# Optimization experiments

Hardware: AMD Instinct MI355X
Metric: run time of the kernel (lower is better)

## Reference

```python
import jax, jax.numpy as jnp
import numpy as np

D_MODEL = 1024
NUM_HEADS = 16
HEAD_DIM = D_MODEL // NUM_HEADS


def setup_inputs() -> dict:
    key = jax.random.key(0)
    k1, k2, k3, k4, k5 = jax.random.split(key, 5)
    scale = 1.0 / np.sqrt(D_MODEL)
    x = jax.random.normal(k1, (2, 2048, D_MODEL), dtype=jnp.float32)
    Wqkv = jax.random.uniform(k2, (D_MODEL, 3 * D_MODEL), jnp.float32, -scale, scale)
    bqkv = jax.random.uniform(k3, (3 * D_MODEL,), jnp.float32, -scale, scale)
    Wout = jax.random.uniform(k4, (D_MODEL, D_MODEL), jnp.float32, -scale, scale)
    bout = jax.random.uniform(k5, (D_MODEL,), jnp.float32, -scale, scale)
    return {"x": x, "Wqkv": Wqkv, "bqkv": bqkv, "Wout": Wout, "bout": bout}


def reference(x, Wqkv, bqkv, Wout, bout):
    B, S, _ = x.shape
    qkv = x @ Wqkv + bqkv                                   # [B, S, 3*D]
    # reshape to [B, S, H, 3*head_dim] then to [B, H, S, 3*head_dim]
    qkv = qkv.reshape(B, S, NUM_HEADS, 3 * HEAD_DIM).transpose(0, 2, 1, 3)
    q, k, v = jnp.split(qkv, 3, axis=-1)                    # each [B, H, S, hd]
    scaled = jnp.einsum("bhqd,bhkd->bhqk", q, k) / jnp.sqrt(jnp.float32(HEAD_DIM))
    attn = jax.nn.softmax(scaled, axis=-1)                  # [B, H, S, S]
    values = jnp.einsum("bhqk,bhkd->bhqd", attn, v)         # [B, H, S, hd]
    values = values.transpose(0, 2, 1, 3).reshape(B, S, D_MODEL)
    return values @ Wout + bout
```

## Files before the change

### kernel.cpp

```cpp
#include <hip/hip_runtime.h>


typedef __attribute__((ext_vector_type(8)))  short short8;
typedef __attribute__((ext_vector_type(4)))  short short4v;
typedef __attribute__((ext_vector_type(8)))  float float8;
typedef __attribute__((ext_vector_type(4)))  float f32x4;
typedef __attribute__((ext_vector_type(16))) float f32x16;
typedef __attribute__((ext_vector_type(4)))  int   int4v;

#define D_MODEL 1024
#define NHEAD   16
#define HD      64
#define SEQ     2048
#define N3      (3*D_MODEL)
#define MB      (1024*1024)

static __device__ __forceinline__ float bf2f(short s) {
    unsigned u = ((unsigned)(unsigned short)s) << 16;
    return __builtin_bit_cast(float, u);
}
static __device__ __forceinline__ short f2bf(float f) {
    unsigned u = __builtin_bit_cast(unsigned, f);
    u = (u + 0x7fff + ((u >> 16) & 1)) >> 16;
    return (short)u;
}
static __device__ __forceinline__ unsigned cvtpk(float a, float b) {
    unsigned r;
    asm("v_cvt_pk_bf16_f32 %0, %1, %2" : "=v"(r) : "v"(a), "v"(b));
    return r;
}
#define PLSWAP(a, b) asm("v_permlane32_swap_b32 %0, %1" : "+v"(a), "+v"(b))

static __device__ __forceinline__ void gl16(const short* g, short* l) {
    __builtin_amdgcn_global_load_lds(
        (const __attribute__((address_space(1))) unsigned int*)g,
        (__attribute__((address_space(3))) unsigned int*)l, 16, 0, 0);
}

__global__ __launch_bounds__(256) void prep(
    const float* __restrict__ x, const float* __restrict__ Wqkv,
    const float* __restrict__ Wout,
    short* __restrict__ Xh, short* __restrict__ Xl,
    short* __restrict__ Wh, short* __restrict__ Wl,
    short* __restrict__ Woh, short* __restrict__ Wol)
{
    __shared__ float tile[32][33];
    const int bid = blockIdx.x;
    const int tid = threadIdx.x;

    if (bid < 2048) {
        const int i = (bid * 256 + tid) * 8;
        const float8 v = *(const float8*)&x[i];
        short8 h, l;
#pragma unroll
        for (int j = 0; j < 8; ++j) {
            h[j] = f2bf(v[j]);
            l[j] = f2bf(v[j] - bf2f(h[j]));
        }
        *(short8*)&Xh[i] = h;
        *(short8*)&Xl[i] = l;
        return;
    }

    const float* in; short *hi, *lo; int K, N, bx, by;
    if (bid < 5120) {
        const int b2 = bid - 2048;
        in = Wqkv; hi = Wh; lo = Wl; K = D_MODEL; N = N3;
        bx = b2 % 96; by = b2 / 96;
    } else {
        const int b3 = bid - 5120;
        in = Wout; hi = Woh; lo = Wol; K = D_MODEL; N = D_MODEL;
        bx = b3 & 31; by = b3 >> 5;
    }
    const int n0 = bx * 32, k0 = by * 32;
    const int tx = tid & 31, ty = tid >> 5;
#pragma unroll
    for (int i = 0; i < 4; ++i)
        tile[ty + 8*i][tx] = in[(k0 + ty + 8*i) * N + (n0 + tx)];
    __syncthreads();
#pragma unroll
    for (int i = 0; i < 4; ++i) {
        const float v  = tile[tx][ty + 8*i];
        const short vh = f2bf(v);
        const short vl = f2bf(v - bf2f(vh));
        const int idx  = (n0 + ty + 8*i) * K + (k0 + tx);
        hi[idx] = vh;
        lo[idx] = vl;
    }
}

#define QBUF_SH 20480
#define OFF_AL  4096
#define OFF_BH  8192
#define OFF_BL  14336

__global__ __launch_bounds__(512, 4) void qkv_gemm8(
    const short* __restrict__ Xh, const short* __restrict__ Xl,
    const short* __restrict__ Bh, const short* __restrict__ Bl,
    const float* __restrict__ bias,
    short* __restrict__ Qo, short* __restrict__ Ko, short* __restrict__ Vt)
{
    __shared__ __attribute__((aligned(16))) short smem[2 * QBUF_SH];

    const int tid  = threadIdx.x;
    const int wave = tid >> 6, lane = tid & 63;
    const int q4 = lane >> 4, l16 = lane & 15;
    const int wr = wave >> 2, wc = wave & 3;
    const int csw = (q4 ^ ((l16 ^ (l16 >> 2)) & 3)) * 8;

    const int flat = blockIdx.x;
    const int sw = (flat & 7) * 64 + (flat >> 3);
    const int mt = sw & 31, nt = sw >> 5;
    const int m0 = mt * 128, n0 = nt * 192;

    const short* srcp[5];
#pragma unroll
    for (int j = 0; j < 5; ++j) {
        const int id = j * 512 + tid;
        int r; const short* mat; int row0;
        if (id < 512)       { r = id >> 2;          mat = Xh; row0 = m0; }
        else if (id < 1024) { r = (id - 512) >> 2;  mat = Xl; row0 = m0; }
        else if (id < 1792) { r = (id - 1024) >> 2; mat = Bh; row0 = n0; }
        else                { r = (id - 1792) >> 2; mat = Bl; row0 = n0; }
        const int cg = (id & 3) ^ ((r ^ (r >> 2)) & 3);
        srcp[j] = &mat[(size_t)(row0 + r) * D_MODEL + cg * 8];
    }

    auto stage = [&](int b) {
#pragma unroll
        for (int j = 0; j < 5; ++j) {
            gl16(srcp[j], smem + b * QBUF_SH + (j * 512 + tid) * 8);
            srcp[j] += 32;
        }
    };

    f32x4 acc[4][3];
#pragma unroll
    for (int i = 0; i < 4; ++i)
#pragma unroll
        for (int j = 0; j < 3; ++j) acc[i][j] = (f32x4){0.f, 0.f, 0.f, 0.f};

    stage(0);
    asm volatile("s_waitcnt vmcnt(0)" ::: "memory");
    __builtin_amdgcn_s_barrier();

    for (int t = 0; t < 32; ++t) {
        const int cur = t & 1;
        const short* base = smem + cur * QBUF_SH;
        const short* Ah_s = base;
        const short* Al_s = base + OFF_AL;
        const short* Bh_s = base + OFF_BH;
        const short* Bl_s = base + OFF_BL;

        short8 bhf[3], blf[3], a0h[2], a0l[2];
#pragma unroll
        for (int n = 0; n < 3; ++n) {
            const int rb = (wc * 48 + n * 16 + l16) * 32 + csw;
            bhf[n] = *(const short8*)(Bh_s + rb);
            blf[n] = *(const short8*)(Bl_s + rb);
        }
#pragma unroll
        for (int ti = 0; ti < 2; ++ti) {
            const int ra = (wr * 64 + ti * 16 + l16) * 32 + csw;
            a0h[ti] = *(const short8*)(Ah_s + ra);
            a0l[ti] = *(const short8*)(Al_s + ra);
        }
        if (t < 31) stage(cur ^ 1);
        __builtin_amdgcn_s_barrier();
        asm volatile("s_waitcnt lgkmcnt(0)" ::: "memory");
        __builtin_amdgcn_sched_barrier(0);
        short8 a1h[2], a1l[2];
#pragma unroll
        for (int ti = 0; ti < 2; ++ti) {
            const int ra = (wr * 64 + (2 + ti) * 16 + l16) * 32 + csw;
            a1h[ti] = *(const short8*)(Ah_s + ra);
            a1l[ti] = *(const short8*)(Al_s + ra);
        }
        __builtin_amdgcn_sched_barrier(0);
        __builtin_amdgcn_s_setprio(1);
#pragma unroll
        for (int ti = 0; ti < 2; ++ti)
#pragma unroll
            for (int n = 0; n < 3; ++n) {
                acc[ti][n] = __builtin_amdgcn_mfma_f32_16x16x32_bf16(a0h[ti], bhf[n], acc[ti][n], 0, 0, 0);
                acc[ti][n] = __builtin_amdgcn_mfma_f32_16x16x32_bf16(a0h[ti], blf[n], acc[ti][n], 0, 0, 0);
                acc[ti][n] = __builtin_amdgcn_mfma_f32_16x16x32_bf16(a0l[ti], bhf[n], acc[ti][n], 0, 0, 0);
            }
        __builtin_amdgcn_s_setprio(0);
        __builtin_amdgcn_s_barrier();

        asm volatile("s_waitcnt lgkmcnt(0)" ::: "memory");
        __builtin_amdgcn_sched_barrier(0);
        __builtin_amdgcn_s_setprio(1);
#pragma unroll
        for (int ti = 0; ti < 2; ++ti)
#pragma unroll
            for (int n = 0; n < 3; ++n) {
                acc[2+ti][n] = __builtin_amdgcn_mfma_f32_16x16x32_bf16(a1h[ti], bhf[n], acc[2+ti][n], 0, 0, 0);
                acc[2+ti][n] = __builtin_amdgcn_mfma_f32_16x16x32_bf16(a1h[ti], blf[n], acc[2+ti][n], 0, 0, 0);
                acc[2+ti][n] = __builtin_amdgcn_mfma_f32_16x16x32_bf16(a1l[ti], bhf[n], acc[2+ti][n], 0, 0, 0);
            }
        __builtin_amdgcn_s_setprio(0);
        asm volatile("s_waitcnt vmcnt(0)" ::: "memory");
        __builtin_amdgcn_s_barrier();
    }

    const float SCALE_Q = 0.125f * 1.4426950408889634f;
#pragma unroll
    for (int tj = 0; tj < 3; ++tj) {
        const int jj = wc * 48 + tj * 16 + l16;
        const int n  = nt * 192 + jj;
        const float bv = bias[n];
#pragma unroll
        for (int ti = 0; ti < 4; ++ti) {
            const int mb = m0 + wr * 64 + ti * 16 + q4 * 4;
            const int b = mb >> 11;
            const int s = mb & 2047;
            const int bh_ = b * NHEAD + nt;
            if (jj >= 128) {
                short4v v4;
#pragma unroll
                for (int r = 0; r < 4; ++r) v4[r] = f2bf(acc[ti][tj][r] + bv);
                *(short4v*)&Vt[(bh_ * HD + (jj - 128)) * SEQ + s] = v4;
            } else if (jj < 64) {
#pragma unroll
                for (int r = 0; r < 4; ++r)
                    Qo[(bh_ * SEQ + s + r) * HD + jj] = f2bf((acc[ti][tj][r] + bv) * SCALE_Q);
            } else {
#pragma unroll
                for (int r = 0; r < 4; ++r)
                    Ko[(bh_ * SEQ + s + r) * HD + (jj - 64)] = f2bf(acc[ti][tj][r] + bv);
            }
        }
    }
}

__global__ __launch_bounds__(256, 2) void attn_tscore(
    const short* __restrict__ Q, const short* __restrict__ K,
    const short* __restrict__ Vt,
    float* __restrict__ Opart, float2* __restrict__ Ml)
{
    __shared__ __attribute__((aligned(16))) char smem[36864];
    short (*Ks)[72] = (short(*)[72])smem;
    short (*Vs)[72] = (short(*)[72])(smem + 18432);

    const int bh  = blockIdx.x;
    const int qb  = blockIdx.y;
    const int kvz = blockIdx.z;

    const short* Qp  = Q  + (size_t)bh * SEQ * HD;
    const short* Kp  = K  + (size_t)bh * SEQ * HD + (size_t)kvz * 1024 * HD;
    const short* Vtp = Vt + (size_t)bh * HD * SEQ + (size_t)kvz * 1024;

    const int tid  = threadIdx.x;
    const int wave = tid >> 6, lane = tid & 63;
    const int l5 = lane & 31, hf = lane >> 5;
    const int q0w = qb * 128 + wave * 32;

    short8 qf[4];
#pragma unroll
    for (int c = 0; c < 4; ++c)
        qf[c] = *(const short8*)&Qp[(q0w + l5) * HD + c * 16 + hf * 8];

    f32x16 oacc0 = (f32x16)(0.f), oacc1 = (f32x16)(0.f);
    float m = -1.0e30f, l = 0.f;

    const int sr = tid >> 2;
    const int sc = (tid & 3) * 16;

    short8 kr0 = *(const short8*)&Kp[sr * HD + sc];
    short8 kr1 = *(const short8*)&Kp[sr * HD + sc + 8];
    short8 vr0 = *(const short8*)&Vtp[sr * SEQ + sc];
    short8 vr1 = *(const short8*)&Vtp[sr * SEQ + sc + 8];
    *(short8*)&Ks[sr][sc]     = kr0;
    *(short8*)&Ks[sr][sc + 8] = kr1;
    *(short8*)&Vs[sr][sc]     = vr0;
    *(short8*)&Vs[sr][sc + 8] = vr1;
    __syncthreads();

    for (int kc = 0; kc < 16; ++kc) {
        const int buf = (kc & 1) << 6;

        if (kc < 15) {
            const int nkb = (kc + 1) << 6;
            kr0 = *(const short8*)&Kp[(nkb + sr) * HD + sc];
            kr1 = *(const short8*)&Kp[(nkb + sr) * HD + sc + 8];
            vr0 = *(const short8*)&Vtp[sr * SEQ + nkb + sc];
            vr1 = *(const short8*)&Vtp[sr * SEQ + nkb + sc + 8];
        }

        f32x16 s0 = (f32x16)(0.f), s1 = (f32x16)(0.f);
#pragma unroll
        for (int c = 0; c < 4; ++c) {
            const short8 ka0 = *(const short8*)&Ks[buf + l5][c * 16 + hf * 8];
            const short8 ka1 = *(const short8*)&Ks[buf + 32 + l5][c * 16 + hf * 8];
            s0 = __builtin_amdgcn_mfma_f32_32x32x16_bf16(ka0, qf[c], s0, 0, 0, 0);
            s1 = __builtin_amdgcn_mfma_f32_32x32x16_bf16(ka1, qf[c], s1, 0, 0, 0);
        }

        float t[8];
#pragma unroll
        for (int i = 0; i < 8; ++i)
            t[i] = fmaxf(fmaxf(s0[i], s0[i + 8]), fmaxf(s1[i], s1[i + 8]));
        float pmax = fmaxf(fmaxf(fmaxf(t[0], t[1]), fmaxf(t[2], t[3])),
                           fmaxf(fmaxf(t[4], t[5]), fmaxf(t[6], t[7])));
        pmax = fmaxf(pmax, __shfl_xor(pmax, 32, 64));

        if (!__all(pmax - m <= 8.0f)) {
            const float mnew  = fmaxf(m, pmax);
            const float alpha = exp2f(m - mnew);
#pragma unroll
            for (int i = 0; i < 16; ++i) { oacc0[i] *= alpha; oacc1[i] *= alpha; }
            l *= alpha;
            m = mnew;
        }

        float p0[16], p1[16];
#pragma unroll
        for (int i = 0; i < 16; ++i) { p0[i] = exp2f(s0[i] - m); p1[i] = exp2f(s1[i] - m); }
        float sa = 0.f, sb = 0.f, sc_ = 0.f, sd = 0.f;
#pragma unroll
        for (int i = 0; i < 4; ++i) {
            sa += p0[i] + p0[i + 8];
            sb += p0[i + 4] + p0[i + 12];
            sc_ += p1[i] + p1[i + 8];
            sd += p1[i + 4] + p1[i + 12];
        }
        float rs = (sa + sb) + (sc_ + sd);
        rs += __shfl_xor(rs, 32, 64);
        l += rs;

        unsigned u0 = cvtpk(p0[0],  p0[1]),  u1 = cvtpk(p0[2],  p0[3]);
        unsigned u2 = cvtpk(p0[4],  p0[5]),  u3 = cvtpk(p0[6],  p0[7]);
        unsigned u4 = cvtpk(p0[8],  p0[9]),  u5 = cvtpk(p0[10], p0[11]);
        unsigned u6 = cvtpk(p0[12], p0[13]), u7 = cvtpk(p0[14], p0[15]);
        unsigned w0 = cvtpk(p1[0],  p1[1]),  w1 = cvtpk(p1[2],  p1[3]);
        unsigned w2 = cvtpk(p1[4],  p1[5]),  w3 = cvtpk(p1[6],  p1[7]);
        unsigned w4 = cvtpk(p1[8],  p1[9]),  w5 = cvtpk(p1[10], p1[11]);
        unsigned w6 = cvtpk(p1[12], p1[13]), w7 = cvtpk(p1[14], p1[15]);
        PLSWAP(u0, u2); PLSWAP(u1, u3); PLSWAP(u4, u6); PLSWAP(u5, u7);
        PLSWAP(w0, w2); PLSWAP(w1, w3); PLSWAP(w4, w6); PLSWAP(w5, w7);
        int4v pb0 = (int4v){ (int)u0, (int)u1, (int)u2, (int)u3 };
        int4v pb1 = (int4v){ (int)u4, (int)u5, (int)u6, (int)u7 };
        int4v pb2 = (int4v){ (int)w0, (int)w1, (int)w2, (int)w3 };
        int4v pb3 = (int4v){ (int)w4, (int)w5, (int)w6, (int)w7 };
        const short8 pbf0 = __builtin_bit_cast(short8, pb0);
        const short8 pbf1 = __builtin_bit_cast(short8, pb1);
        const short8 pbf2 = __builtin_bit_cast(short8, pb2);
        const short8 pbf3 = __builtin_bit_cast(short8, pb3);

        {
            const short8 va0 = *(const short8*)&Vs[buf + l5][hf * 8];
            const short8 va1 = *(const short8*)&Vs[buf + l5][16 + hf * 8];
            const short8 va2 = *(const short8*)&Vs[buf + l5][32 + hf * 8];
            const short8 va3 = *(const short8*)&Vs[buf + l5][48 + hf * 8];
            oacc0 = __builtin_amdgcn_mfma_f32_32x32x16_bf16(va0, pbf0, oacc0, 0, 0, 0);
            oacc0 = __builtin_amdgcn_mfma_f32_32x32x16_bf16(va1, pbf1, oacc0, 0, 0, 0);
            oacc0 = __builtin_amdgcn_mfma_f32_32x32x16_bf16(va2, pbf2, oacc0, 0, 0, 0);
            oacc0 = __builtin_amdgcn_mfma_f32_32x32x16_bf16(va3, pbf3, oacc0, 0, 0, 0);
            const short8 vb0 = *(const short8*)&Vs[buf + 32 + l5][hf * 8];
            const short8 vb1 = *(const short8*)&Vs[buf + 32 + l5][16 + hf * 8];
            const short8 vb2 = *(const short8*)&Vs[buf + 32 + l5][32 + hf * 8];
            const short8 vb3 = *(const short8*)&Vs[buf + 32 + l5][48 + hf * 8];
            oacc1 = __builtin_amdgcn_mfma_f32_32x32x16_bf16(vb0, pbf0, oacc1, 0, 0, 0);
            oacc1 = __builtin_amdgcn_mfma_f32_32x32x16_bf16(vb1, pbf1, oacc1, 0, 0, 0);
            oacc1 = __builtin_amdgcn_mfma_f32_32x32x16_bf16(vb2, pbf2, oacc1, 0, 0, 0);
            oacc1 = __builtin_amdgcn_mfma_f32_32x32x16_bf16(vb3, pbf3, oacc1, 0, 0, 0);
        }

        if (kc < 15) {
            const int wb = ((kc + 1) & 1) << 6;
            *(short8*)&Ks[wb + sr][sc]     = kr0;
            *(short8*)&Ks[wb + sr][sc + 8] = kr1;
            *(short8*)&Vs[wb + sr][sc]     = vr0;
            *(short8*)&Vs[wb + sr][sc + 8] = vr1;
        }
        __syncthreads();
    }

    float* Op = Opart + ((((size_t)kvz * 32 + bh) * 16 + qb) * 4 + wave) * 2048;
#pragma unroll
    for (int r = 0; r < 4; ++r) {
        float4 v;
        v.x = oacc0[4*r]; v.y = oacc0[4*r+1]; v.z = oacc0[4*r+2]; v.w = oacc0[4*r+3];
        *(float4*)&Op[r * 256 + lane * 4] = v;
    }
#pragma unroll
    for (int r = 0; r < 4; ++r) {
        float4 v;
        v.x = oacc1[4*r]; v.y = oacc1[4*r+1]; v.z = oacc1[4*r+2]; v.w = oacc1[4*r+3];
        *(float4*)&Op[(4 + r) * 256 + lane * 4] = v;
    }
    if (hf == 0) {
        float2 mv; mv.x = m; mv.y = l;
        Ml[((size_t)kvz * 32 + bh) * 2048 + q0w + l5] = mv;
    }
}

__global__ __launch_bounds__(256) void attn_merge(
    const float* __restrict__ Opart, const float2* __restrict__ Ml,
    short* __restrict__ Ch, short* __restrict__ Cl)
{
    __shared__ float epi[4][32][68];
    const int tid = threadIdx.x, wave = tid >> 6, lane = tid & 63;
    const int l5 = lane & 31, hf = lane >> 5;
    const int task = blockIdx.x * 4 + wave;
    const int bh = task >> 6;
    const int qb = (task >> 2) & 15;
    const int wq = task & 3;
    const int bi = bh >> 4, hi_ = bh & 15;
    const int q0w = qb * 128 + wq * 32;

    const float2 v0 = Ml[(size_t)bh * 2048 + q0w + l5];
    const float2 v1 = Ml[((size_t)32 + bh) * 2048 + q0w + l5];
    const float M  = fmaxf(v0.x, v1.x);
    const float w0 = exp2f(v0.x - M), w1 = exp2f(v1.x - M);
    const float inv = 1.0f / (v0.y * w0 + v1.y * w1);
    const float f0 = w0 * inv, f1 = w1 * inv;

    const float* Op0 = Opart + (((size_t)bh * 16 + qb) * 4 + wq) * 2048;
    const float* Op1 = Opart + ((((size_t)32 + bh) * 16 + qb) * 4 + wq) * 2048;
    float o[32];
#pragma unroll
    for (int r = 0; r < 8; ++r) {
        const float4 a = *(const float4*)&Op0[r * 256 + lane * 4];
        const float4 b = *(const float4*)&Op1[r * 256 + lane * 4];
        o[4*r]   = a.x * f0 + b.x * f1;
        o[4*r+1] = a.y * f0 + b.y * f1;
        o[4*r+2] = a.z * f0 + b.z * f1;
        o[4*r+3] = a.w * f0 + b.w * f1;
    }
#pragma unroll
    for (int r = 0; r < 16; ++r) {
        const int d = (r & 3) + 8 * (r >> 2) + 4 * hf;
        epi[wave][l5][d]      = o[r];
        epi[wave][l5][32 + d] = o[16 + r];
    }
    __builtin_amdgcn_s_waitcnt(0);
#pragma unroll
    for (int pass = 0; pass < 8; ++pass) {
        const int row = pass * 4 + (lane >> 4);
        const int col = (lane & 15) * 4;
        const float4 v = *(const float4*)&epi[wave][row][col];
        const float ov[4] = {v.x, v.y, v.z, v.w};
        short4v hh, ll;
#pragma unroll
        for (int i = 0; i < 4; ++i) {
            hh[i] = f2bf(ov[i]);
            ll[i] = f2bf(ov[i] - bf2f(hh[i]));
        }
        const size_t co = ((size_t)(bi * SEQ + q0w + row)) * D_MODEL + hi_ * HD + col;
        *(short4v*)&Ch[co] = hh;
        *(short4v*)&Cl[co] = ll;
    }
}

#define OBUF_SH 12288
#define OO_AL   4096
#define OO_BH   8192
#define OO_BL   10240

__global__ __launch_bounds__(256, 4) void out_gemm2(
    const short* __restrict__ Ah, const short* __restrict__ Al,
    const short* __restrict__ Bh, const short* __restrict__ Bl,
    const float* __restrict__ bias, float* __restrict__ out)
{
    __shared__ __attribute__((aligned(16))) short smem[2 * OBUF_SH];

    const int tid  = threadIdx.x;
    const int wave = tid >> 6, lane = tid & 63;
    const int q4 = lane >> 4, l16 = lane & 15;
    const int wr = wave >> 1, wc = wave & 1;
    const int csw = (q4 ^ ((l16 ^ (l16 >> 2)) & 3)) * 8;

    const int flat = blockIdx.x;
    const int sw = (flat & 7) * 64 + (flat >> 3);
    const int mt = sw & 31, nt = sw >> 5;
    const int m0 = mt * 128, n0 = nt * 64;

    const short* srcp[6];
#pragma unroll
    for (int j = 0; j < 6; ++j) {
        const int id = j * 256 + tid;
        int r; const short* mat; int row0;
        if (id < 512)       { r = id >> 2;          mat = Ah; row0 = m0; }
        else if (id < 1024) { r = (id - 512) >> 2;  mat = Al; row0 = m0; }
        else if (id < 1280) { r = (id - 1024) >> 2; mat = Bh; row0 = n0; }
        else                { r = (id - 1280) >> 2; mat = Bl; row0 = n0; }
        const int cg = (id & 3) ^ ((r ^ (r >> 2)) & 3);
        srcp[j] = &mat[(size_t)(row0 + r) * D_MODEL + cg * 8];
    }

    auto stage = [&](int b) {
#pragma unroll
        for (int j = 0; j < 6; ++j) {
            gl16(srcp[j], smem + b * OBUF_SH + (j * 256 + tid) * 8);
            srcp[j] += 32;
        }
    };

    f32x4 acc[4][2];
#pragma unroll
    for (int i = 0; i < 4; ++i)
#pragma unroll
        for (int j = 0; j < 2; ++j) acc[i][j] = (f32x4){0.f, 0.f, 0.f, 0.f};

    stage(0);
    asm volatile("s_waitcnt vmcnt(0)" ::: "memory");
    __builtin_amdgcn_s_barrier();

    for (int t = 0; t < 32; ++t) {
        const int cur = t & 1;
        const short* base = smem + cur * OBUF_SH;
        const short* Ah_s = base;
        const short* Al_s = base + OO_AL;
        const short* Bh_s = base + OO_BH;
        const short* Bl_s = base + OO_BL;

        short8 bhf[2], blf[2], a0h[2], a0l[2];
#pragma unroll
        for (int n = 0; n < 2; ++n) {
            const int rb = (wc * 32 + n * 16 + l16) * 32 + csw;
            bhf[n] = *(const short8*)(Bh_s + rb);
            blf[n] = *(const short8*)(Bl_s + rb);
        }
#pragma unroll
        for (int ti = 0; ti < 2; ++ti) {
            const int ra = (wr * 64 + ti * 16 + l16) * 32 + csw;
            a0h[ti] = *(const short8*)(Ah_s + ra);
            a0l[ti] = *(const short8*)(Al_s + ra);
        }
        if (t < 31) stage(cur ^ 1);
        __builtin_amdgcn_s_barrier();
        asm volatile("s_waitcnt lgkmcnt(0)" ::: "memory");
        __builtin_amdgcn_sched_barrier(0);
        short8 a1h[2], a1l[2];
#pragma unroll
        for (int ti = 0; ti < 2; ++ti) {
            const int ra = (wr * 64 + (2 + ti) * 16 + l16) * 32 + csw;
            a1h[ti] = *(const short8*)(Ah_s + ra);
            a1l[ti] = *(const short8*)(Al_s + ra);
        }
        __builtin_amdgcn_sched_barrier(0);
        __builtin_amdgcn_s_setprio(1);
#pragma unroll
        for (int ti = 0; ti < 2; ++ti)
#pragma unroll
            for (int n = 0; n < 2; ++n) {
                acc[ti][n] = __builtin_amdgcn_mfma_f32_16x16x32_bf16(a0h[ti], bhf[n], acc[ti][n], 0, 0, 0);
                acc[ti][n] = __builtin_amdgcn_mfma_f32_16x16x32_bf16(a0h[ti], blf[n], acc[ti][n], 0, 0, 0);
                acc[ti][n] = __builtin_amdgcn_mfma_f32_16x16x32_bf16(a0l[ti], bhf[n], acc[ti][n], 0, 0, 0);
            }
        __builtin_amdgcn_s_setprio(0);
        __builtin_amdgcn_s_barrier();

        asm volatile("s_waitcnt lgkmcnt(0)" ::: "memory");
        __builtin_amdgcn_sched_barrier(0);
        __builtin_amdgcn_s_setprio(1);
#pragma unroll
        for (int ti = 0; ti < 2; ++ti)
#pragma unroll
            for (int n = 0; n < 2; ++n) {
                acc[2+ti][n] = __builtin_amdgcn_mfma_f32_16x16x32_bf16(a1h[ti], bhf[n], acc[2+ti][n], 0, 0, 0);
                acc[2+ti][n] = __builtin_amdgcn_mfma_f32_16x16x32_bf16(a1h[ti], blf[n], acc[2+ti][n], 0, 0, 0);
                acc[2+ti][n] = __builtin_amdgcn_mfma_f32_16x16x32_bf16(a1l[ti], bhf[n], acc[2+ti][n], 0, 0, 0);
            }
        __builtin_amdgcn_s_setprio(0);
        asm volatile("s_waitcnt vmcnt(0)" ::: "memory");
        __builtin_amdgcn_s_barrier();
    }

#pragma unroll
    for (int tj = 0; tj < 2; ++tj) {
        const int n = n0 + wc * 32 + tj * 16 + l16;
        const float bv = bias[n];
#pragma unroll
        for (int ti = 0; ti < 4; ++ti) {
            const int mb = m0 + wr * 64 + ti * 16 + q4 * 4;
#pragma unroll
            for (int r = 0; r < 4; ++r)
                out[(size_t)(mb + r) * D_MODEL + n] = acc[ti][tj][r] + bv;
        }
    }
}

extern "C" void kernel_launch(void* const* d_in, const int* in_sizes, int n_in,
                              void* d_out, int out_size, void* d_ws, size_t ws_size,
                              hipStream_t stream)
{
    const float* x    = (const float*)d_in[0];
    const float* Wqkv = (const float*)d_in[1];
    const float* bqkv = (const float*)d_in[2];
    const float* Wout = (const float*)d_in[3];
    const float* bout = (const float*)d_in[4];
    float* out = (float*)d_out;

    char* ws = (char*)d_ws;
    short*  Woh   = (short*)(ws);
    short*  Wol   = (short*)(ws +  2*MB);
    short*  Qb    = (short*)(ws +  4*MB);
    short*  Kb    = (short*)(ws + 12*MB);
    short*  Vtb   = (short*)(ws + 20*MB);
    float*  Opart = (float*)(ws + 28*MB);
    float2* Ml    = (float2*)(ws + 60*MB);
    short*  Ch    = (short*)(ws +  4*MB);
    short*  Cl    = (short*)(ws + 12*MB);
    short*  Xh    = (short*)(ws + 28*MB);
    short*  Xl    = (short*)(ws + 36*MB);
    short*  Wh    = (short*)(ws + 44*MB);
    short*  Wl    = (short*)(ws + 50*MB);

    prep<<<6144, 256, 0, stream>>>(x, Wqkv, Wout, Xh, Xl, Wh, Wl, Woh, Wol);
    qkv_gemm8<<<dim3(512), 512, 0, stream>>>(Xh, Xl, Wh, Wl, bqkv, Qb, Kb, Vtb);
    attn_tscore<<<dim3(32, 16, 2), 256, 0, stream>>>(Qb, Kb, Vtb, Opart, Ml);
    attn_merge<<<512, 256, 0, stream>>>(Opart, Ml, Ch, Cl);
    out_gemm2<<<dim3(512), 256, 0, stream>>>(Ch, Cl, Woh, Wol, bout, out);
}
```

Baseline: 263.3 us.

## Fold max subtraction into MFMA seed and compute row sums via ones-MFMA

```diff
diff --git a/kernel.cpp b/kernel.cpp
--- a/kernel.cpp
+++ b/kernel.cpp
@@ -262,8 +262,14 @@
     for (int c = 0; c < 4; ++c)
         qf[c] = *(const short8*)&Qp[(q0w + l5) * HD + c * 16 + hf * 8];
 
+    short8 one8;
+#pragma unroll
+    for (int i = 0; i < 8; ++i) one8[i] = (short)0x3F80;
+
     f32x16 oacc0 = (f32x16)(0.f), oacc1 = (f32x16)(0.f);
-    float m = -1.0e30f, l = 0.f;
+    f32x16 lacc  = (f32x16)(0.f);
+    f32x16 mseed = (f32x16)(0.f);
+    float m = 0.f;
 
     const int sr = tid >> 2;
     const int sc = (tid & 3) * 16;
@@ -289,9 +295,15 @@
             vr1 = *(const short8*)&Vtp[sr * SEQ + nkb + sc + 8];
         }
 
-        f32x16 s0 = (f32x16)(0.f), s1 = (f32x16)(0.f);
-#pragma unroll
-        for (int c = 0; c < 4; ++c) {
+        f32x16 s0, s1;
+        {
+            const short8 ka0 = *(const short8*)&Ks[buf + l5][hf * 8];
+            const short8 ka1 = *(const short8*)&Ks[buf + 32 + l5][hf * 8];
+            s0 = __builtin_amdgcn_mfma_f32_32x32x16_bf16(ka0, qf[0], mseed, 0, 0, 0);
+            s1 = __builtin_amdgcn_mfma_f32_32x32x16_bf16(ka1, qf[0], mseed, 0, 0, 0);
+        }
+#pragma unroll
+        for (int c = 1; c < 4; ++c) {
             const short8 ka0 = *(const short8*)&Ks[buf + l5][c * 16 + hf * 8];
             const short8 ka1 = *(const short8*)&Ks[buf + 32 + l5][c * 16 + hf * 8];
             s0 = __builtin_amdgcn_mfma_f32_32x32x16_bf16(ka0, qf[c], s0, 0, 0, 0);
@@ -306,29 +318,23 @@
                            fmaxf(fmaxf(t[4], t[5]), fmaxf(t[6], t[7])));
         pmax = fmaxf(pmax, __shfl_xor(pmax, 32, 64));
 
-        if (!__all(pmax - m <= 8.0f)) {
-            const float mnew  = fmaxf(m, pmax);
-            const float alpha = exp2f(m - mnew);
-#pragma unroll
-            for (int i = 0; i < 16; ++i) { oacc0[i] *= alpha; oacc1[i] *= alpha; }
-            l *= alpha;
-            m = mnew;
+        if (!__all(pmax <= 8.0f)) {
+            const float delta = fmaxf(pmax, 0.0f);
+            const float alpha = exp2f(-delta);
+#pragma unroll
+            for (int i = 0; i < 16; ++i) {
+                oacc0[i] *= alpha; oacc1[i] *= alpha; lacc[i] *= alpha;
+            }
+            m += delta;
+#pragma unroll
+            for (int i = 0; i < 16; ++i) mseed[i] = -m;
+#pragma unroll
+            for (int i = 0; i < 16; ++i) { s0[i] -= delta; s1[i] -= delta; }
         }
 
         float p0[16], p1[16];
 #pragma unroll
-        for (int i = 0; i < 16; ++i) { p0[i] = exp2f(s0[i] - m); p1[i] = exp2f(s1[i] - m); }
-        float sa = 0.f, sb = 0.f, sc_ = 0.f, sd = 0.f;
-#pragma unroll
-        for (int i = 0; i < 4; ++i) {
-            sa += p0[i] + p0[i + 8];
-            sb += p0[i + 4] + p0[i + 12];
-            sc_ += p1[i] + p1[i + 8];
-            sd += p1[i + 4] + p1[i + 12];
-        }
-        float rs = (sa + sb) + (sc_ + sd);
-        rs += __shfl_xor(rs, 32, 64);
-        l += rs;
+        for (int i = 0; i < 16; ++i) { p0[i] = exp2f(s0[i]); p1[i] = exp2f(s1[i]); }
 
         unsigned u0 = cvtpk(p0[0],  p0[1]),  u1 = cvtpk(p0[2],  p0[3]);
         unsigned u2 = cvtpk(p0[4],  p0[5]),  u3 = cvtpk(p0[6],  p0[7]);
@@ -366,6 +372,10 @@
             oacc1 = __builtin_amdgcn_mfma_f32_32x32x16_bf16(vb1, pbf1, oacc1, 0, 0, 0);
             oacc1 = __builtin_amdgcn_mfma_f32_32x32x16_bf16(vb2, pbf2, oacc1, 0, 0, 0);
             oacc1 = __builtin_amdgcn_mfma_f32_32x32x16_bf16(vb3, pbf3, oacc1, 0, 0, 0);
+            lacc  = __builtin_amdgcn_mfma_f32_32x32x16_bf16(one8, pbf0, lacc, 0, 0, 0);
+            lacc  = __builtin_amdgcn_mfma_f32_32x32x16_bf16(one8, pbf1, lacc, 0, 0, 0);
+            lacc  = __builtin_amdgcn_mfma_f32_32x32x16_bf16(one8, pbf2, lacc, 0, 0, 0);
+            lacc  = __builtin_amdgcn_mfma_f32_32x32x16_bf16(one8, pbf3, lacc, 0, 0, 0);
         }
 
         if (kc < 15) {
@@ -392,7 +402,7 @@
         *(float4*)&Op[(4 + r) * 256 + lane * 4] = v;
     }
     if (hf == 0) {
-        float2 mv; mv.x = m; mv.y = l;
+        float2 mv; mv.x = m; mv.y = lacc[0];
         Ml[((size_t)kvz * 32 + bh) * 2048 + q0w + l5] = mv;
     }
 }
```

Result: no change. 264.5 us (+0.5%).
